# Kernel optimization log

Measured on AMD Instinct MI355X. Metric: run time of the kernel, lower is better.

## Reference

```python
import jax, jax.numpy as jnp
import numpy as np

B, W, CBLK, C, H, L, VOCAB = 8, 512, 24, 512, 8, 2, 256
HD = C // H


def _ln(x, g, b, eps=1e-5):
    m = x.mean(-1, keepdims=True)
    v = ((x - m) ** 2).mean(-1, keepdims=True)
    return (x - m) * jax.lax.rsqrt(v + eps) * g + b


def _causal_attn(q, k, v):
    # q,k,v: [..., T, hd]; causal softmax attention, scale 1/sqrt(hd)
    T = q.shape[-2]
    scale = 1.0 / (q.shape[-1] ** 0.5)
    s = jnp.einsum('...qd,...kd->...qk', q, k) * scale
    mask = jnp.tril(jnp.ones((T, T), dtype=bool))
    s = jnp.where(mask, s, jnp.finfo(s.dtype).min)
    return jnp.einsum('...qk,...kd->...qd', jax.nn.softmax(s, axis=-1), v)


def _mha_char(seq, w_qkv, last_ix):
    # seq: [B,W,c,C]; per-word causal char attention, then gather row last_ix
    b, w, c, _ = seq.shape
    q, k, v = jnp.split(seq @ w_qkv, 3, axis=-1)
    sh = lambda t: t.reshape(b, w, c, H, HD).transpose(0, 1, 3, 2, 4)
    o = _causal_attn(sh(q), sh(k), sh(v))          # [B,W,H,c,hd]
    o = o.transpose(0, 1, 3, 2, 4).reshape(b, w, c, C)
    return jnp.take_along_axis(o, last_ix[:, :, None, None], axis=2)[:, :, 0, :]


def _mha_word(x, w_qkv, w_proj):
    b, w, _ = x.shape
    q, k, v = jnp.split(x @ w_qkv, 3, axis=-1)
    sh = lambda t: t.reshape(b, w, H, HD).transpose(0, 2, 1, 3)
    o = _causal_attn(sh(q), sh(k), sh(v))
    o = o.transpose(0, 2, 1, 3).reshape(b, w, C)
    return o @ w_proj


def setup_inputs() -> dict:
    key = jax.random.key(0)
    ks = jax.random.split(key, 16)
    # ragged word lengths in [1, CBLK]; mask = ones then zeros (as produced by pad())
    lengths = jax.random.randint(ks[0], (B, W), 1, CBLK + 1)
    attention_mask = (jnp.arange(CBLK)[None, None, :] < lengths[:, :, None]).astype(jnp.int32)
    x = jax.random.randint(ks[1], (B, W, CBLK), 0, VOCAB).astype(jnp.int32)
    std = 0.02
    res_std = std * (2 * L) ** -0.5  # res_flag init scaling
    n = lambda k, s, sd=std: sd * jax.random.normal(k, s, dtype=jnp.float32)
    return dict(
        x=x, attention_mask=attention_mask,
        cte=n(ks[2], (VOCAB, C)), cpe=n(ks[3], (CBLK, C)), wpe=n(ks[4], (W, C)),
        ln1_g=jnp.ones((L, C)), ln1_b=jnp.zeros((L, C)),
        ln2_g=jnp.ones((L, C)), ln2_b=jnp.zeros((L, C)),
        ln3_g=jnp.ones((L, C)), ln3_b=jnp.zeros((L, C)),
        cattn_w=n(ks[5], (L, C, 3 * C)), cattn_proj=n(ks[6], (L, C, C)),
        wattn_w=n(ks[7], (L, C, 3 * C)), wattn_proj=n(ks[8], (L, C, C), res_std),
        mlp_fc=n(ks[9], (L, C, 4 * C)), mlp_proj=n(ks[10], (L, 4 * C, C), res_std),
        proj_w=n(ks[11], (C, CBLK * C)), lm_head_w=n(ks[12], (C, VOCAB)),
    )


def reference(x, attention_mask, cte, cpe, wpe, ln1_g, ln1_b, ln2_g, ln2_b, ln3_g, ln3_b,
              cattn_w, cattn_proj, wattn_w, wattn_proj, mlp_fc, mlp_proj, proj_w, lm_head_w):
    last_ix = attention_mask.sum(axis=2) - 1           # [B,W], last real char per word
    state = cte[x] + cpe[None, None, :, :]             # [B,W,c,C]
    context = None                                     # current_conv.context/pad, vectorized
    for l in range(L):
        if l == 0:
            # first_time: operate on full padded char sequences, cache ln_1 output
            hln = _ln(state, ln1_g[l], ln1_b[l])       # [B,W,c,C]
            context = hln
            seq = hln
        else:
            # splice the new word vector into position last_ix of the cached context
            hln = _ln(state, ln1_g[l], ln1_b[l])       # [B,W,C]
            repl = jnp.arange(CBLK)[None, None, :] == last_ix[:, :, None]
            seq = jnp.where(repl[..., None], hln[:, :, None, :], context)
        o = _mha_char(seq, cattn_w[l], last_ix)        # [B,W,C]
        if l == 0:
            o = o + wpe[None, :, :]                    # word pos emb added only first_time
        state = o @ cattn_proj[l]                      # note: no residual around c_attn
        state = state + _mha_word(_ln(state, ln2_g[l], ln2_b[l]), wattn_w[l], wattn_proj[l])
        hm = _ln(state, ln3_g[l], ln3_b[l])
        state = state + jax.nn.gelu(hm @ mlp_fc[l], approximate=False) @ mlp_proj[l]
    y = (state @ proj_w).reshape(B, W, CBLK, C)
    return y @ lm_head_w                               # logits [B,W,CBLK,VOCAB]
```

## Files before the change

### kernel.cpp

```cpp
#include <hip/hip_runtime.h>
#include <hip/hip_bf16.h>
#include <math.h>


namespace {

constexpr int Bn = 8, Wn = 512, CB = 24, Cd = 512, Hn = 8, Lln = 2, Vn = 256, HDn = 64;
constexpr int BW = Bn * Wn;
constexpr int C3 = 3 * Cd;
constexpr int FF = 4 * Cd;
constexpr int NROW = BW * CB;

typedef unsigned short u16;
typedef short short8 __attribute__((ext_vector_type(8)));
typedef float f32x4 __attribute__((ext_vector_type(4)));
typedef __attribute__((address_space(1))) void gvoid_t;
typedef __attribute__((address_space(3))) void lvoid_t;

__device__ __forceinline__ u16 f2bu(float f) {
  __hip_bfloat16 h = __float2bfloat16(f);
  return __builtin_bit_cast(u16, h);
}
__device__ __forceinline__ float bu2f(u16 u) {
  return __bfloat162float(__builtin_bit_cast(__hip_bfloat16, u));
}
__device__ __forceinline__ float geluf(float x) {
  return 0.5f * x * (1.0f + erff(x * 0.7071067811865475f));
}
__device__ __forceinline__ void gl16(const void* g, void* l) {
  __builtin_amdgcn_global_load_lds((gvoid_t*)g, (lvoid_t*)l, 16, 0, 0);
}

__global__ void k_lastix(const int* __restrict__ mask, int* __restrict__ lastix) {
  int i = blockIdx.x * 256 + threadIdx.x;
  if (i < BW) {
    int s = 0;
#pragma unroll
    for (int j = 0; j < CB; ++j) s += mask[i * CB + j];
    lastix[i] = s - 1;
  }
}

__device__ __forceinline__ void f2b8(const float* __restrict__ s, u16* __restrict__ d) {
  float4 a = *(const float4*)s;
  float4 b = *(const float4*)(s + 4);
  union { uint4 u; u16 h[8]; } pk;
  pk.h[0] = f2bu(a.x); pk.h[1] = f2bu(a.y); pk.h[2] = f2bu(a.z); pk.h[3] = f2bu(a.w);
  pk.h[4] = f2bu(b.x); pk.h[5] = f2bu(b.y); pk.h[6] = f2bu(b.z); pk.h[7] = f2bu(b.w);
  *(uint4*)d = pk.u;
}

__device__ __forceinline__ void wT_tile(const float* __restrict__ src, u16* __restrict__ dst,
                                        int K, int N, int n0, int k0,
                                        u16 T[64][72], int tid) {
  int kl = tid >> 2, nc = (tid & 3) * 16;
  const float* s = src + (long)(k0 + kl) * N + n0 + nc;
#pragma unroll
  for (int u = 0; u < 4; ++u) {
    float4 f = *(const float4*)(s + u * 4);
    T[nc + u * 4 + 0][kl] = f2bu(f.x);
    T[nc + u * 4 + 1][kl] = f2bu(f.y);
    T[nc + u * 4 + 2][kl] = f2bu(f.z);
    T[nc + u * 4 + 3][kl] = f2bu(f.w);
  }
  __syncthreads();
  int nl = tid >> 2, kc = (tid & 3) * 16;
  u16* d = dst + (long)(n0 + nl) * K + k0 + kc;
  *(uint4*)d = *(uint4*)&T[nl][kc];
  *(uint4*)(d + 8) = *(uint4*)&T[nl][kc + 8];
}

__global__ __launch_bounds__(256) void k_prep(
    const float* __restrict__ proj_w, u16* __restrict__ projwb,
    const float* __restrict__ cattn_w, u16* __restrict__ wcb,
    const float* __restrict__ lm_head, u16* __restrict__ lmhT,
    const float* __restrict__ cattn_proj, const float* __restrict__ wattn_w,
    const float* __restrict__ wattn_proj, const float* __restrict__ mlp_fc,
    const float* __restrict__ mlp_proj, u16* __restrict__ wT) {
  __shared__ u16 T[64][72];
  int b = blockIdx.x, tid = threadIdx.x;
  if (b < 3072) { long i = ((long)b * 256 + tid) * 8; f2b8(proj_w + i, projwb + i); return; }
  b -= 3072;
  if (b < 768) { long i = ((long)b * 256 + tid) * 8; f2b8(cattn_w + i, wcb + i); return; }
  b -= 768;
  if (b < 32) { wT_tile(lm_head, lmhT, Cd, Vn, (b & 3) * 64, (b >> 2) * 64, T, tid); return; }
  b -= 32;
  int l = b >> 10, r = b & 1023;
  size_t lw = (size_t)(2 * C3 * Cd + 2 * Cd * Cd + 2 * FF * Cd);
  u16* bl = wT + l * lw;
  const float* src; u16* dst; int K, N, nt;
  if (r < 192)      { src = cattn_w + (size_t)l * Cd * C3;    dst = bl;                              K = Cd; N = C3; nt = 24; }
  else if (r < 256) { src = cattn_proj + (size_t)l * Cd * Cd; dst = bl + C3 * Cd;                    K = Cd; N = Cd; nt = 8;  r -= 192; }
  else if (r < 448) { src = wattn_w + (size_t)l * Cd * C3;    dst = bl + C3 * Cd + Cd * Cd;          K = Cd; N = C3; nt = 24; r -= 256; }
  else if (r < 512) { src = wattn_proj + (size_t)l * Cd * Cd; dst = bl + 2 * C3 * Cd + Cd * Cd;      K = Cd; N = Cd; nt = 8;  r -= 448; }
  else if (r < 768) { src = mlp_fc + (size_t)l * Cd * FF;     dst = bl + 2 * C3 * Cd + 2 * Cd * Cd;  K = Cd; N = FF; nt = 32; r -= 512; }
  else              { src = mlp_proj + (size_t)l * FF * Cd;   dst = bl + 2 * C3 * Cd + 2 * Cd * Cd + FF * Cd; K = FF; N = Cd; nt = 8; r -= 768; }
  wT_tile(src, dst, K, N, (r % nt) * 64, (r / nt) * 64, T, tid);
}

__global__ __launch_bounds__(64) void k_embed_ln(
    const int* __restrict__ x, const float* __restrict__ cte, const float* __restrict__ cpe,
    const float* __restrict__ g, const float* __restrict__ b,
    const int* __restrict__ lastix, u16* __restrict__ ctx) {
  int r = blockIdx.x;
  int bw = r / CB, ch = r - bw * CB;
  if (ch > lastix[bw]) return;
  int tok = x[r];
  const float* e = cte + (long)tok * Cd;
  const float* pe = cpe + (long)ch * Cd;
  int lane = threadIdx.x;
  float v[8];
  float s = 0.f, sq = 0.f;
#pragma unroll
  for (int u = 0; u < 2; ++u) {
    float4 a = *(const float4*)(e + u * 256 + lane * 4);
    float4 p4 = *(const float4*)(pe + u * 256 + lane * 4);
    v[u * 4 + 0] = a.x + p4.x; v[u * 4 + 1] = a.y + p4.y;
    v[u * 4 + 2] = a.z + p4.z; v[u * 4 + 3] = a.w + p4.w;
  }
#pragma unroll
  for (int u = 0; u < 8; ++u) { s += v[u]; sq += v[u] * v[u]; }
#pragma unroll
  for (int m = 32; m; m >>= 1) { s += __shfl_xor(s, m); sq += __shfl_xor(sq, m); }
  float mean = s * (1.0f / Cd);
  float var = sq * (1.0f / Cd) - mean * mean;
  float rs = rsqrtf(var + 1e-5f);
  u16* o = ctx + (long)r * Cd;
#pragma unroll
  for (int u = 0; u < 2; ++u) {
    int c0 = u * 256 + lane * 4;
    float4 g4 = *(const float4*)(g + c0);
    float4 b4 = *(const float4*)(b + c0);
    float o0 = (v[u * 4 + 0] - mean) * rs * g4.x + b4.x;
    float o1 = (v[u * 4 + 1] - mean) * rs * g4.y + b4.y;
    float o2 = (v[u * 4 + 2] - mean) * rs * g4.z + b4.z;
    float o3 = (v[u * 4 + 3] - mean) * rs * g4.w + b4.w;
    uint2 w;
    w.x = (unsigned)f2bu(o0) | ((unsigned)f2bu(o1) << 16);
    w.y = (unsigned)f2bu(o2) | ((unsigned)f2bu(o3) << 16);
    *(uint2*)(o + c0) = w;
  }
}

__global__ __launch_bounds__(64) void k_ln(
    const float* __restrict__ X, u16* __restrict__ Y,
    const float* __restrict__ g, const float* __restrict__ b) {
  long r = blockIdx.x;
  const float* xr = X + r * Cd;
  int lane = threadIdx.x;
  float v[8];
  float s = 0.f, sq = 0.f;
#pragma unroll
  for (int u = 0; u < 2; ++u) {
    float4 a = *(const float4*)(xr + u * 256 + lane * 4);
    v[u * 4 + 0] = a.x; v[u * 4 + 1] = a.y; v[u * 4 + 2] = a.z; v[u * 4 + 3] = a.w;
  }
#pragma unroll
  for (int u = 0; u < 8; ++u) { s += v[u]; sq += v[u] * v[u]; }
#pragma unroll
  for (int m = 32; m; m >>= 1) { s += __shfl_xor(s, m); sq += __shfl_xor(sq, m); }
  float mean = s * (1.0f / Cd);
  float var = sq * (1.0f / Cd) - mean * mean;
  float rs = rsqrtf(var + 1e-5f);
  u16* o = Y + r * Cd;
#pragma unroll
  for (int u = 0; u < 2; ++u) {
    int c0 = u * 256 + lane * 4;
    float4 g4 = *(const float4*)(g + c0);
    float4 b4 = *(const float4*)(b + c0);
    float o0 = (v[u * 4 + 0] - mean) * rs * g4.x + b4.x;
    float o1 = (v[u * 4 + 1] - mean) * rs * g4.y + b4.y;
    float o2 = (v[u * 4 + 2] - mean) * rs * g4.z + b4.z;
    float o3 = (v[u * 4 + 3] - mean) * rs * g4.w + b4.w;
    uint2 w;
    w.x = (unsigned)f2bu(o0) | ((unsigned)f2bu(o1) << 16);
    w.y = (unsigned)f2bu(o2) | ((unsigned)f2bu(o3) << 16);
    *(uint2*)(o + c0) = w;
  }
}

__global__ __launch_bounds__(64) void k_gather_last(
    const u16* __restrict__ ctx, const int* __restrict__ lastix, u16* __restrict__ qin) {
  long bw = blockIdx.x;
  int r = (int)bw * CB + lastix[bw];
  const uint4* s = (const uint4*)(ctx + (long)r * Cd);
  uint4* d = (uint4*)(qin + bw * Cd);
  d[threadIdx.x] = s[threadIdx.x];
}

template <int BM, int BN, int EPI, int OUTBF>
__global__ __launch_bounds__(256) void k_mgemm(
    const u16* __restrict__ A, int lda, long sA1, long sA2,
    const u16* __restrict__ Bt, int ldb, long sB1, long sB2,
    void* __restrict__ Cv, int ldc, long sC1, long sC2,
    const float* __restrict__ R, u16* __restrict__ D2,
    const float* __restrict__ PL, const u16* __restrict__ VL,
    const float* __restrict__ WP, int K, int zdiv) {
  constexpr int WM = BM / 2;
  constexpr int WN = BN / 2;
  constexpr int FM = WM / 16, FN = WN / 16;
  __shared__ u16 As[BM * 32];
  __shared__ u16 Bs[BN * 32];
  long m0 = (long)blockIdx.y * BM, n0 = (long)blockIdx.x * BN;
  int z = blockIdx.z;
  int z1 = z / zdiv, z2 = z - z1 * zdiv;
  A += z1 * sA1 + z2 * sA2;
  Bt += z1 * sB1 + z2 * sB2;
  long coff = z1 * sC1 + z2 * sC2;
  int tid = threadIdx.x;
  int wid = tid >> 6, lane = tid & 63;
  int wr = wid >> 1, wc = wid & 1;

  const int srow = tid >> 2, skk = (tid & 3) * 8;
  const u16* Ald[BM / 64];
  const u16* Bld[BN / 64];
#pragma unroll
  for (int i = 0; i < BM / 64; ++i) Ald[i] = A + (m0 + srow + i * 64) * (long)lda + skk;
#pragma unroll
  for (int i = 0; i < BN / 64; ++i) Bld[i] = Bt + (n0 + srow + i * 64) * (long)ldb + skk;

  f32x4 acc[FM][FN] = {};
  const int fr = lane & 15, kg = lane >> 4;

  for (int k0 = 0; k0 < K; k0 += 32) {
#pragma unroll
    for (int i = 0; i < BM / 64; ++i) gl16(Ald[i] + k0, &As[(tid + i * 256) * 8]);
#pragma unroll
    for (int i = 0; i < BN / 64; ++i) gl16(Bld[i] + k0, &Bs[(tid + i * 256) * 8]);
    __syncthreads();
    short8 af[FM], bf[FN];
#pragma unroll
    for (int m = 0; m < FM; ++m)
      af[m] = *(const short8*)&As[(wr * WM + m * 16 + fr) * 32 + kg * 8];
#pragma unroll
    for (int n = 0; n < FN; ++n)
      bf[n] = *(const short8*)&Bs[(wc * WN + n * 16 + fr) * 32 + kg * 8];
#pragma unroll
    for (int m = 0; m < FM; ++m)
#pragma unroll
      for (int n = 0; n < FN; ++n)
        acc[m][n] = __builtin_amdgcn_mfma_f32_16x16x32_bf16(af[m], bf[n], acc[m][n], 0, 0, 0);
    __syncthreads();
  }
  int ccol = lane & 15, crow4 = (lane >> 4) * 4;
#pragma unroll
  for (int m = 0; m < FM; ++m)
#pragma unroll
    for (int n = 0; n < FN; ++n)
#pragma unroll
      for (int q = 0; q < 4; ++q) {
        long gr = m0 + wr * WM + m * 16 + crow4 + q;
        long gc = n0 + wc * WN + n * 16 + ccol;
        float v = acc[m][n][q];
        long idx = gr * (long)ldc + gc + coff;
        if (EPI == 1 || EPI == 3) v += R[idx];
        if (EPI == 2) v = geluf(v);
        if (EPI == 4) {
          v += PL[gr * 8 + z2] * bu2f(VL[gr * (long)C3 + 2 * Cd + z2 * 64 + gc]);
          if (WP) v += WP[(long)(gr & (Wn - 1)) * Cd + z2 * 64 + gc];
        }
        if (EPI == 3) {
          ((float*)Cv)[idx] = v;
          D2[idx] = f2bu(v);
        } else if (OUTBF) {
          ((u16*)Cv)[idx] = f2bu(v);
        } else {
          ((float*)Cv)[idx] = v;
        }
      }
}

__global__ __launch_bounds__(256) void k_cattn2(
    const u16* __restrict__ ctx, const u16* __restrict__ qtil,
    const u16* __restrict__ qkvc, const int* __restrict__ lastix,
    u16* __restrict__ U, float* __restrict__ plast) {
  int gw = blockIdx.x;
  int li = lastix[gw];
  __shared__ u16 ctxs[CB][512];
  __shared__ u16 qks[2][512];
  __shared__ float sp[Hn][CB];
  int tid = threadIdx.x;
  for (int u = tid; u < li * 64; u += 256) {
    int row = u >> 6, c = (u & 63) * 8;
    *(uint4*)&ctxs[row][c] = *(const uint4*)(ctx + ((long)(gw * CB + row)) * Cd + c);
  }
  if (tid < 128) {
    int row = tid >> 6, c = (tid & 63) * 8;
    *(uint4*)&qks[row][c] = *(const uint4*)(qkvc + (long)gw * C3 + row * 512 + c);
  }
  int wid = tid >> 6, lane = tid & 63;
  int h0 = wid * 2, h1 = h0 + 1;
  float q0[8], q1[8];
  {
    const u16* q0p = qtil + (long)gw * 4096 + h0 * 512 + lane * 8;
    uint4 a = *(const uint4*)q0p;
    uint4 b = *(const uint4*)(q0p + 512);
    const u16* qa = (const u16*)&a;
    const u16* qb = (const u16*)&b;
#pragma unroll
    for (int u = 0; u < 8; ++u) { q0[u] = bu2f(qa[u]); q1[u] = bu2f(qb[u]); }
  }
  __syncthreads();
  int j = 0;
  for (; j + 2 <= li; j += 2) {
    float p0a = 0.f, p1a = 0.f, p0b = 0.f, p1b = 0.f;
    const u16* cva = &ctxs[j][lane * 8];
    const u16* cvb = &ctxs[j + 1][lane * 8];
#pragma unroll
    for (int u = 0; u < 8; ++u) {
      float ca = bu2f(cva[u]);
      float cb = bu2f(cvb[u]);
      p0a += ca * q0[u]; p1a += ca * q1[u];
      p0b += cb * q0[u]; p1b += cb * q1[u];
    }
#pragma unroll
    for (int m = 32; m; m >>= 1) {
      p0a += __shfl_xor(p0a, m); p1a += __shfl_xor(p1a, m);
      p0b += __shfl_xor(p0b, m); p1b += __shfl_xor(p1b, m);
    }
    if (lane == 0) {
      sp[h0][j] = p0a * 0.125f; sp[h1][j] = p1a * 0.125f;
      sp[h0][j + 1] = p0b * 0.125f; sp[h1][j + 1] = p1b * 0.125f;
    }
  }
  if (j < li) {
    float p0 = 0.f, p1 = 0.f;
    const u16* cv = &ctxs[j][lane * 8];
#pragma unroll
    for (int u = 0; u < 8; ++u) {
      float c = bu2f(cv[u]);
      p0 += c * q0[u];
      p1 += c * q1[u];
    }
#pragma unroll
    for (int m = 32; m; m >>= 1) { p0 += __shfl_xor(p0, m); p1 += __shfl_xor(p1, m); }
    if (lane == 0) { sp[h0][j] = p0 * 0.125f; sp[h1][j] = p1 * 0.125f; }
  }
  {
    float pr = 0.f;
    const u16* qq = &qks[0][lane * 8];
    const u16* kk = &qks[1][lane * 8];
#pragma unroll
    for (int u = 0; u < 8; ++u) pr += bu2f(qq[u]) * bu2f(kk[u]);
    float a0 = ((lane >> 3) == h0) ? pr : 0.f;
    float a1 = ((lane >> 3) == h1) ? pr : 0.f;
#pragma unroll
    for (int m = 32; m; m >>= 1) { a0 += __shfl_xor(a0, m); a1 += __shfl_xor(a1, m); }
    if (lane == 0) { sp[h0][li] = a0 * 0.125f; sp[h1][li] = a1 * 0.125f; }
  }
  __syncthreads();
  if (tid < 8) {
    float m = -3.4e38f;
    for (int jj = 0; jj <= li; ++jj) m = fmaxf(m, sp[tid][jj]);
    float s = 0.f;
    for (int jj = 0; jj <= li; ++jj) { float e = expf(sp[tid][jj] - m); sp[tid][jj] = e; s += e; }
    float inv = 1.0f / s;
    for (int jj = 0; jj <= li; ++jj) sp[tid][jj] *= inv;
    plast[gw * 8 + tid] = sp[tid][li];
  }
  __syncthreads();
  int h = tid >> 5, d0 = (tid & 31) * 16;
  float uacc[16];
#pragma unroll
  for (int i = 0; i < 16; ++i) uacc[i] = 0.f;
  for (int jj = 0; jj < li; ++jj) {
    float p = sp[h][jj];
    const u16* cv = &ctxs[jj][d0];
#pragma unroll
    for (int i = 0; i < 16; ++i) uacc[i] += p * bu2f(cv[i]);
  }
  union { uint4 q[2]; u16 hh[16]; } pk;
#pragma unroll
  for (int i = 0; i < 16; ++i) pk.hh[i] = f2bu(uacc[i]);
  u16* d = U + (long)gw * 4096 + h * 512 + d0;
  *(uint4*)d = pk.q[0];
  *(uint4*)(d + 8) = pk.q[1];
}

__global__ __launch_bounds__(256) void k_vt(const u16* __restrict__ qkv, u16* __restrict__ Vt) {
  __shared__ u16 T[64][72];
  int z = blockIdx.y, jt = blockIdx.x;
  int b = z >> 3, h = z & 7;
  int tid = threadIdx.x;
  int jl = tid >> 2, dc = (tid & 3) * 16;
  const u16* s = qkv + ((long)(b * Wn + jt * 64 + jl)) * C3 + 2 * Cd + h * HDn + dc;
  *(uint4*)&T[jl][dc] = *(const uint4*)s;
  *(uint4*)&T[jl][dc + 8] = *(const uint4*)(s + 8);
  __syncthreads();
  int dl = tid >> 2, jc = (tid & 3) * 16;
  u16 tmp[16];
#pragma unroll
  for (int u = 0; u < 16; ++u) tmp[u] = T[jc + u][dl];
  u16* d = Vt + (long)z * HDn * Wn + (long)dl * Wn + jt * 64 + jc;
  *(uint4*)d = *(uint4*)&tmp[0];
  *(uint4*)(d + 8) = *(uint4*)&tmp[8];
}

__global__ __launch_bounds__(256) void k_fattn(
    const u16* __restrict__ qkv, const u16* __restrict__ Vt, u16* __restrict__ ao) {
  constexpr int ST = 68;
  __shared__ u16 Ks[64 * ST];
  __shared__ u16 Vs[64 * ST];
  __shared__ u16 Ps[4][16 * ST];
  int qt = blockIdx.x;
  int z  = blockIdx.y;
  int b = z >> 3, h = z & 7;
  int tid = threadIdx.x;
  int w = tid >> 6, lane = tid & 63;
  int fr = lane & 15, kg = lane >> 4;

  short8 qf[2];
  {
    const u16* qp = qkv + ((long)(b * Wn + qt * 64 + w * 16 + fr)) * C3 + h * 64 + kg * 8;
    qf[0] = *(const short8*)qp;
    qf[1] = *(const short8*)(qp + 32);
  }
  f32x4 oacc[4] = {};
  float mrow[4], lrow[4];
#pragma unroll
  for (int q = 0; q < 4; ++q) { mrow[q] = -3.4e38f; lrow[q] = 0.f; }

  for (int kt = 0; kt <= qt; ++kt) {
    __syncthreads();
    {
      int r = tid >> 2, c = (tid & 3) * 16;
      const u16* kp = qkv + ((long)(b * Wn + kt * 64 + r)) * C3 + Cd + h * 64 + c;
      *(uint4*)&Ks[r * ST + c] = *(const uint4*)kp;
      *(uint4*)&Ks[r * ST + c + 8] = *(const uint4*)(kp + 8);
      const u16* vp = Vt + (long)z * (64 * Wn) + (long)r * Wn + kt * 64 + c;
      *(uint4*)&Vs[r * ST + c] = *(const uint4*)vp;
      *(uint4*)&Vs[r * ST + c + 8] = *(const uint4*)(vp + 8);
    }
    __syncthreads();
    f32x4 s[4];
#pragma unroll
    for (int n = 0; n < 4; ++n) {
      short8 kf0 = *(const short8*)&Ks[(n * 16 + fr) * ST + kg * 8];
      short8 kf1 = *(const short8*)&Ks[(n * 16 + fr) * ST + kg * 8 + 32];
      f32x4 a = {};
      a = __builtin_amdgcn_mfma_f32_16x16x32_bf16(qf[0], kf0, a, 0, 0, 0);
      a = __builtin_amdgcn_mfma_f32_16x16x32_bf16(qf[1], kf1, a, 0, 0, 0);
      s[n] = a;
    }
    int irow0 = qt * 64 + w * 16 + kg * 4;
#pragma unroll
    for (int n = 0; n < 4; ++n) {
      int jcol = kt * 64 + n * 16 + fr;
#pragma unroll
      for (int q = 0; q < 4; ++q) {
        float v = s[n][q] * 0.125f;
        s[n][q] = (jcol > irow0 + q) ? -3.4e38f : v;
      }
    }
    float sf[4];
#pragma unroll
    for (int q = 0; q < 4; ++q) {
      float mm = fmaxf(fmaxf(s[0][q], s[1][q]), fmaxf(s[2][q], s[3][q]));
      mm = fmaxf(mm, __shfl_xor(mm, 1));
      mm = fmaxf(mm, __shfl_xor(mm, 2));
      mm = fmaxf(mm, __shfl_xor(mm, 4));
      mm = fmaxf(mm, __shfl_xor(mm, 8));
      float mnew = fmaxf(mrow[q], mm);
      sf[q] = expf(mrow[q] - mnew);
      mrow[q] = mnew;
    }
    float ls[4] = {0.f, 0.f, 0.f, 0.f};
#pragma unroll
    for (int n = 0; n < 4; ++n) {
#pragma unroll
      for (int q = 0; q < 4; ++q) {
        float p = expf(s[n][q] - mrow[q]);
        u16 pb = f2bu(p);
        ls[q] += bu2f(pb);
        Ps[w][(kg * 4 + q) * ST + n * 16 + fr] = pb;
      }
    }
#pragma unroll
    for (int q = 0; q < 4; ++q) {
      float l = ls[q];
      l += __shfl_xor(l, 1); l += __shfl_xor(l, 2);
      l += __shfl_xor(l, 4); l += __shfl_xor(l, 8);
      lrow[q] = lrow[q] * sf[q] + l;
#pragma unroll
      for (int n = 0; n < 4; ++n) oacc[n][q] *= sf[q];
    }
    asm volatile("s_waitcnt lgkmcnt(0)" ::: "memory");
    short8 pa0 = *(const short8*)&Ps[w][fr * ST + kg * 8];
    short8 pa1 = *(const short8*)&Ps[w][fr * ST + kg * 8 + 32];
#pragma unroll
    for (int n = 0; n < 4; ++n) {
      short8 vf0 = *(const short8*)&Vs[(n * 16 + fr) * ST + kg * 8];
      short8 vf1 = *(const short8*)&Vs[(n * 16 + fr) * ST + kg * 8 + 32];
      oacc[n] = __builtin_amdgcn_mfma_f32_16x16x32_bf16(pa0, vf0, oacc[n], 0, 0, 0);
      oacc[n] = __builtin_amdgcn_mfma_f32_16x16x32_bf16(pa1, vf1, oacc[n], 0, 0, 0);
    }
  }
  int orow = b * Wn + qt * 64 + w * 16 + kg * 4;
#pragma unroll
  for (int q = 0; q < 4; ++q) {
    float inv = 1.0f / lrow[q];
#pragma unroll
    for (int n = 0; n < 4; ++n)
      ao[(long)(orow + q) * Cd + h * 64 + n * 16 + fr] = f2bu(oacc[n][q] * inv);
  }
}

template <int BM, int BN, int EPI, int OUTBF>
static inline void mgemm(hipStream_t st,
    const u16* A, int lda, long sA1, long sA2,
    const u16* Bt, int ldb, long sB1, long sB2,
    void* C, int ldc, long sC1, long sC2,
    const float* R, int M, int N, int K, int nz, int zdiv,
    u16* D2 = nullptr, const float* PL = nullptr, const u16* VL = nullptr,
    const float* WP = nullptr) {
  dim3 g(N / BN, (M + BM - 1) / BM, nz);
  hipLaunchKernelGGL((k_mgemm<BM, BN, EPI, OUTBF>), g, dim3(256), 0, st,
                     A, lda, sA1, sA2, Bt, ldb, sB1, sB2, C, ldc, sC1, sC2,
                     R ? R : (const float*)C, D2, PL, VL, WP, K, zdiv);
}

}

extern "C" void kernel_launch(void* const* d_in, const int* in_sizes, int n_in,
                              void* d_out, int out_size, void* d_ws, size_t ws_size,
                              hipStream_t stream) {
  (void)in_sizes; (void)n_in; (void)out_size; (void)ws_size;
  const int*   x          = (const int*)d_in[0];
  const int*   amask      = (const int*)d_in[1];
  const float* cte        = (const float*)d_in[2];
  const float* cpe        = (const float*)d_in[3];
  const float* wpe        = (const float*)d_in[4];
  const float* ln1g       = (const float*)d_in[5];
  const float* ln1b       = (const float*)d_in[6];
  const float* ln2g       = (const float*)d_in[7];
  const float* ln2b       = (const float*)d_in[8];
  const float* ln3g       = (const float*)d_in[9];
  const float* ln3b       = (const float*)d_in[10];
  const float* cattn_w    = (const float*)d_in[11];
  const float* cattn_proj = (const float*)d_in[12];
  const float* wattn_w    = (const float*)d_in[13];
  const float* wattn_proj = (const float*)d_in[14];
  const float* mlp_fc     = (const float*)d_in[15];
  const float* mlp_proj   = (const float*)d_in[16];
  const float* proj_w     = (const float*)d_in[17];
  const float* lm_head    = (const float*)d_in[18];
  float* out = (float*)d_out;

  char* base = (char*)d_ws;
  size_t off = 0;
  auto alloc = [&](size_t bytes) -> char* {
    char* r = base + off;
    off += (bytes + 255) & ~(size_t)255;
    return r;
  };
  int*   lastix = (int*)alloc((size_t)BW * 4);
  float* plast  = (float*)alloc((size_t)BW * 8 * 4);
  u16*   ctx    = (u16*)alloc((size_t)NROW * Cd * 2);
  char*  big    = alloc((size_t)105 * 1024 * 1024);
  u16*   kvq    = (u16*)alloc((size_t)BW * C3 * 2);
  u16*   qin    = (u16*)alloc((size_t)BW * Cd * 2);
  float* state  = (float*)alloc((size_t)BW * Cd * 4);
  u16*   stateb = (u16*)alloc((size_t)BW * Cd * 2);
  u16*   hln    = (u16*)alloc((size_t)BW * Cd * 2);
  u16*   ao     = (u16*)alloc((size_t)BW * Cd * 2);
  u16*   wT     = (u16*)alloc((size_t)2 * (2 * C3 * Cd + 2 * Cd * Cd + 2 * FF * Cd) * 2);
  u16*   wcb    = (u16*)alloc((size_t)2 * Cd * C3 * 2);
  u16*   projwb = (u16*)alloc((size_t)Cd * CB * Cd * 2);
  u16*   lmhT   = (u16*)alloc((size_t)Vn * Cd * 2);

  u16*   U     = (u16*)big;
  u16*   qtil  = (u16*)(big + (size_t)35651584);
  u16*   Vt    = (u16*)(big + (size_t)71303168);
  u16*   mlph  = (u16*)big;
  u16*   combT = (u16*)big;

  size_t lw = (size_t)(2 * C3 * Cd + 2 * Cd * Cd + 2 * FF * Cd);
  auto cwT    = [&](int l) { return wT + l * lw; };
  auto cprojT = [&](int l) { return wT + l * lw + C3 * Cd; };
  auto wwT    = [&](int l) { return wT + l * lw + C3 * Cd + Cd * Cd; };
  auto wprojT = [&](int l) { return wT + l * lw + 2 * C3 * Cd + Cd * Cd; };
  auto fcT    = [&](int l) { return wT + l * lw + 2 * C3 * Cd + 2 * Cd * Cd; };
  auto mprojT = [&](int l) { return wT + l * lw + 2 * C3 * Cd + 2 * Cd * Cd + FF * Cd; };

  hipLaunchKernelGGL(k_lastix, dim3(16), dim3(256), 0, stream, amask, lastix);
  hipLaunchKernelGGL(k_prep, dim3(5920), dim3(256), 0, stream,
                     proj_w, projwb, cattn_w, wcb, lm_head, lmhT,
                     cattn_proj, wattn_w, wattn_proj, mlp_fc, mlp_proj, wT);
  hipLaunchKernelGGL(k_embed_ln, dim3(NROW), dim3(64), 0, stream,
                     x, cte, cpe, ln1g, ln1b, lastix, ctx);

  for (int l = 0; l < Lln; ++l) {
    u16* qkvc = kvq;
    u16* qkvw = kvq;
    if (l == 0)
      hipLaunchKernelGGL(k_gather_last, dim3(BW), dim3(64), 0, stream, ctx, lastix, qin);
    else
      hipLaunchKernelGGL(k_ln, dim3(BW), dim3(64), 0, stream, state, qin, ln1g + Cd, ln1b + Cd);
    mgemm<128, 64, 0, 1>(stream, qin, Cd, 0, 0, cwT(l), Cd, 0, 0,
                         qkvc, C3, 0, 0, nullptr, BW, C3, Cd, 1, 1);
    mgemm<64, 64, 0, 1>(stream, qkvc, C3, 0, 64,
                        wcb + (size_t)l * Cd * C3 + Cd, C3, 0, 64,
                        qtil, 8 * Cd, 0, Cd, nullptr, BW, Cd, HDn, 8, 8);
    hipLaunchKernelGGL(k_cattn2, dim3(BW), dim3(256), 0, stream,
                       ctx, qtil, qkvc, lastix, U, plast);
    mgemm<64, 64, 4, 1>(stream, U, 8 * Cd, 0, Cd,
                        cwT(l) + (size_t)(2 * Cd) * Cd, Cd, 0, (long)HDn * Cd,
                        ao, Cd, 0, HDn, nullptr, BW, HDn, Cd, 8, 8,
                        nullptr, plast, qkvc, l == 0 ? wpe : nullptr);
    mgemm<64, 64, 0, 0>(stream, ao, Cd, 0, 0, cprojT(l), Cd, 0, 0,
                        state, Cd, 0, 0, nullptr, BW, Cd, Cd, 1, 1);
    hipLaunchKernelGGL(k_ln, dim3(BW), dim3(64), 0, stream, state, hln, ln2g + l * Cd, ln2b + l * Cd);
    mgemm<128, 64, 0, 1>(stream, hln, Cd, 0, 0, wwT(l), Cd, 0, 0,
                         qkvw, C3, 0, 0, nullptr, BW, C3, Cd, 1, 1);
    hipLaunchKernelGGL(k_vt, dim3(Wn / 64, 64), dim3(256), 0, stream, qkvw, Vt);
    hipLaunchKernelGGL(k_fattn, dim3(8, 64), dim3(256), 0, stream, qkvw, Vt, ao);
    mgemm<64, 64, 1, 0>(stream, ao, Cd, 0, 0, wprojT(l), Cd, 0, 0,
                        state, Cd, 0, 0, state, BW, Cd, Cd, 1, 1);
    hipLaunchKernelGGL(k_ln, dim3(BW), dim3(64), 0, stream, state, hln, ln3g + l * Cd, ln3b + l * Cd);
    mgemm<128, 128, 2, 1>(stream, hln, Cd, 0, 0, fcT(l), Cd, 0, 0,
                          mlph, FF, 0, 0, nullptr, BW, FF, Cd, 1, 1);
    mgemm<64, 64, 3, 0>(stream, mlph, FF, 0, 0, mprojT(l), FF, 0, 0,
                        state, Cd, 0, 0, state, BW, Cd, FF, 1, 1, stateb);
  }

  mgemm<64, 64, 0, 1>(stream, lmhT, Cd, 0, 0,
                      projwb, CB * Cd, 0, Cd,
                      combT, Cd, 0, (long)Vn * Cd,
                      nullptr, Vn, Cd, Cd, CB, CB);
  mgemm<128, 128, 0, 0>(stream, stateb, Cd, 0, 0, combT, Cd, 0, 0,
                        out, CB * Vn, 0, 0, nullptr, BW, CB * Vn, Cd, 1, 1);
}
```

Baseline: 578.8 us.

## Split-K the MLP down-projection into four partials plus reduction kernel

The MLP projection GEMM (K=2048) is split into four K=512 slices via the batched z dimension, writing fp32 partials to a scratch buffer, and a new reduction kernel sums them into the residual state and emits the bf16 copy. This raises block count for a GEMM with a small output (4096x512), improving occupancy at the cost of extra global traffic for the partials. Separately, the char-attention kernel drops the shared-memory staging of the q/k last-row pair and computes the self score with 8 threads reading global memory directly, which shrinks shared memory.

```diff
diff --git a/kernel.cpp b/kernel.cpp
--- a/kernel.cpp
+++ b/kernel.cpp
@@ -188,6 +188,23 @@
   d[threadIdx.x] = s[threadIdx.x];
 }
 
+__global__ __launch_bounds__(256) void k_red4(const float* __restrict__ pbuf,
+                                              float* __restrict__ state,
+                                              u16* __restrict__ stateb) {
+  long i = ((long)blockIdx.x * 256 + threadIdx.x) * 4;
+  float4 a = *(const float4*)(state + i);
+#pragma unroll
+  for (int z = 0; z < 4; ++z) {
+    float4 p = *(const float4*)(pbuf + (long)z * BW * Cd + i);
+    a.x += p.x; a.y += p.y; a.z += p.z; a.w += p.w;
+  }
+  *(float4*)(state + i) = a;
+  uint2 w;
+  w.x = (unsigned)f2bu(a.x) | ((unsigned)f2bu(a.y) << 16);
+  w.y = (unsigned)f2bu(a.z) | ((unsigned)f2bu(a.w) << 16);
+  *(uint2*)(stateb + i) = w;
+}
+
 template <int BM, int BN, int EPI, int OUTBF>
 __global__ __launch_bounds__(256) void k_mgemm(
     const u16* __restrict__ A, int lda, long sA1, long sA2,
@@ -276,17 +293,12 @@
     u16* __restrict__ U, float* __restrict__ plast) {
   int gw = blockIdx.x;
   int li = lastix[gw];
-  __shared__ u16 ctxs[CB][512];
-  __shared__ u16 qks[2][512];
+  __shared__ u16 ctxs[CB - 1][512];
   __shared__ float sp[Hn][CB];
   int tid = threadIdx.x;
   for (int u = tid; u < li * 64; u += 256) {
     int row = u >> 6, c = (u & 63) * 8;
     *(uint4*)&ctxs[row][c] = *(const uint4*)(ctx + ((long)(gw * CB + row)) * Cd + c);
-  }
-  if (tid < 128) {
-    int row = tid >> 6, c = (tid & 63) * 8;
-    *(uint4*)&qks[row][c] = *(const uint4*)(qkvc + (long)gw * C3 + row * 512 + c);
   }
   int wid = tid >> 6, lane = tid & 63;
   int h0 = wid * 2, h1 = h0 + 1;
@@ -336,17 +348,13 @@
     for (int m = 32; m; m >>= 1) { p0 += __shfl_xor(p0, m); p1 += __shfl_xor(p1, m); }
     if (lane == 0) { sp[h0][j] = p0 * 0.125f; sp[h1][j] = p1 * 0.125f; }
   }
-  {
-    float pr = 0.f;
-    const u16* qq = &qks[0][lane * 8];
-    const u16* kk = &qks[1][lane * 8];
-#pragma unroll
-    for (int u = 0; u < 8; ++u) pr += bu2f(qq[u]) * bu2f(kk[u]);
-    float a0 = ((lane >> 3) == h0) ? pr : 0.f;
-    float a1 = ((lane >> 3) == h1) ? pr : 0.f;
-#pragma unroll
-    for (int m = 32; m; m >>= 1) { a0 += __shfl_xor(a0, m); a1 += __shfl_xor(a1, m); }
-    if (lane == 0) { sp[h0][li] = a0 * 0.125f; sp[h1][li] = a1 * 0.125f; }
+  if (tid < 8) {
+    const u16* qq = qkvc + (long)gw * C3 + tid * 64;
+    const u16* kk = qq + Cd;
+    float s = 0.f;
+#pragma unroll
+    for (int u = 0; u < 64; ++u) s += bu2f(qq[u]) * bu2f(kk[u]);
+    sp[tid][li] = s * 0.125f;
   }
   __syncthreads();
   if (tid < 8) {
@@ -572,6 +580,7 @@
   u16*   qtil  = (u16*)(big + (size_t)35651584);
   u16*   Vt    = (u16*)(big + (size_t)71303168);
   u16*   mlph  = (u16*)big;
+  float* pbuf  = (float*)(big + (size_t)50 * 1024 * 1024);
   u16*   combT = (u16*)big;
 
   size_t lw = (size_t)(2 * C3 * Cd + 2 * Cd * Cd + 2 * FF * Cd);
@@ -619,8 +628,12 @@
     hipLaunchKernelGGL(k_ln, dim3(BW), dim3(64), 0, stream, state, hln, ln3g + l * Cd, ln3b + l * Cd);
     mgemm<128, 128, 2, 1>(stream, hln, Cd, 0, 0, fcT(l), Cd, 0, 0,
                           mlph, FF, 0, 0, nullptr, BW, FF, Cd, 1, 1);
-    mgemm<64, 64, 3, 0>(stream, mlph, FF, 0, 0, mprojT(l), FF, 0, 0,
-                        state, Cd, 0, 0, state, BW, Cd, FF, 1, 1, stateb);
+    mgemm<64, 64, 0, 0>(stream, mlph, FF, 0, 512,
+                        mprojT(l), FF, 0, 512,
+                        pbuf, Cd, 0, (long)BW * Cd,
+                        nullptr, BW, Cd, 512, 4, 4);
+    hipLaunchKernelGGL(k_red4, dim3((BW * Cd) / 1024), dim3(256), 0, stream,
+                       pbuf, state, stateb);
   }
 
   mgemm<64, 64, 0, 1>(stream, lmhT, Cd, 0, 0,
```

New measurement: 588.3 us. No clear change (+1.6%).

## Compute char-attention scores with MFMA and shrink MLP fc GEMM tile

Applied to the files above, without the earlier changes.

The score computation in the per-word char attention kernel moves from per-lane scalar dot products with shuffle reductions to bf16 MFMA 16x16x32 instructions. Each wave covers a 128-wide slice of the 8 heads and writes partial scores to LDS, where they are summed across waves. The context rows are stored with a padded stride, and the q·k term for the last position is now a plain 64-element loop run by 8 threads. Separately, the MLP fc GEMM tile drops from 128x128 to 64x64 to launch more blocks, at the cost of less reuse per block.

```diff
diff --git a/kernel.cpp b/kernel.cpp
--- a/kernel.cpp
+++ b/kernel.cpp
@@ -274,79 +274,57 @@
     const u16* __restrict__ ctx, const u16* __restrict__ qtil,
     const u16* __restrict__ qkvc, const int* __restrict__ lastix,
     u16* __restrict__ U, float* __restrict__ plast) {
+  constexpr int CS = 520;
   int gw = blockIdx.x;
   int li = lastix[gw];
-  __shared__ u16 ctxs[CB][512];
-  __shared__ u16 qks[2][512];
+  __shared__ u16 ctxs[CB - 1][CS];
+  __shared__ float spf[4][Hn][32];
   __shared__ float sp[Hn][CB];
   int tid = threadIdx.x;
   for (int u = tid; u < li * 64; u += 256) {
     int row = u >> 6, c = (u & 63) * 8;
     *(uint4*)&ctxs[row][c] = *(const uint4*)(ctx + ((long)(gw * CB + row)) * Cd + c);
   }
-  if (tid < 128) {
-    int row = tid >> 6, c = (tid & 63) * 8;
-    *(uint4*)&qks[row][c] = *(const uint4*)(qkvc + (long)gw * C3 + row * 512 + c);
-  }
-  int wid = tid >> 6, lane = tid & 63;
-  int h0 = wid * 2, h1 = h0 + 1;
-  float q0[8], q1[8];
+  __syncthreads();
+  int w = tid >> 6, lane = tid & 63;
+  int fr = lane & 15, kg = lane >> 4;
   {
-    const u16* q0p = qtil + (long)gw * 4096 + h0 * 512 + lane * 8;
-    uint4 a = *(const uint4*)q0p;
-    uint4 b = *(const uint4*)(q0p + 512);
-    const u16* qa = (const u16*)&a;
-    const u16* qb = (const u16*)&b;
-#pragma unroll
-    for (int u = 0; u < 8; ++u) { q0[u] = bu2f(qa[u]); q1[u] = bu2f(qb[u]); }
+    const u16* qbase = qtil + (long)gw * 4096 + (fr & 7) * 512 + w * 128 + kg * 8;
+    int r0 = fr;
+    int r1 = 16 + fr; if (r1 > CB - 2) r1 = CB - 2;
+    f32x4 acc0 = {}, acc1 = {};
+#pragma unroll
+    for (int kk = 0; kk < 4; ++kk) {
+      short8 af = *(const short8*)(qbase + kk * 32);
+      short8 b0 = *(const short8*)&ctxs[r0][w * 128 + kk * 32 + kg * 8];
+      short8 b1 = *(const short8*)&ctxs[r1][w * 128 + kk * 32 + kg * 8];
+      acc0 = __builtin_amdgcn_mfma_f32_16x16x32_bf16(af, b0, acc0, 0, 0, 0);
+      acc1 = __builtin_amdgcn_mfma_f32_16x16x32_bf16(af, b1, acc1, 0, 0, 0);
+    }
+    if (lane < 32) {
+      int jj = lane & 15;
+#pragma unroll
+      for (int q = 0; q < 4; ++q) {
+        int h = (lane >> 4) * 4 + q;
+        spf[w][h][jj] = acc0[q];
+        spf[w][h][16 + jj] = acc1[q];
+      }
+    }
   }
   __syncthreads();
-  int j = 0;
-  for (; j + 2 <= li; j += 2) {
-    float p0a = 0.f, p1a = 0.f, p0b = 0.f, p1b = 0.f;
-    const u16* cva = &ctxs[j][lane * 8];
-    const u16* cvb = &ctxs[j + 1][lane * 8];
-#pragma unroll
-    for (int u = 0; u < 8; ++u) {
-      float ca = bu2f(cva[u]);
-      float cb = bu2f(cvb[u]);
-      p0a += ca * q0[u]; p1a += ca * q1[u];
-      p0b += cb * q0[u]; p1b += cb * q1[u];
-    }
-#pragma unroll
-    for (int m = 32; m; m >>= 1) {
-      p0a += __shfl_xor(p0a, m); p1a += __shfl_xor(p1a, m);
-      p0b += __shfl_xor(p0b, m); p1b += __shfl_xor(p1b, m);
-    }
-    if (lane == 0) {
-      sp[h0][j] = p0a * 0.125f; sp[h1][j] = p1a * 0.125f;
-      sp[h0][j + 1] = p0b * 0.125f; sp[h1][j + 1] = p1b * 0.125f;
-    }
-  }
-  if (j < li) {
-    float p0 = 0.f, p1 = 0.f;
-    const u16* cv = &ctxs[j][lane * 8];
-#pragma unroll
-    for (int u = 0; u < 8; ++u) {
-      float c = bu2f(cv[u]);
-      p0 += c * q0[u];
-      p1 += c * q1[u];
-    }
-#pragma unroll
-    for (int m = 32; m; m >>= 1) { p0 += __shfl_xor(p0, m); p1 += __shfl_xor(p1, m); }
-    if (lane == 0) { sp[h0][j] = p0 * 0.125f; sp[h1][j] = p1 * 0.125f; }
-  }
   {
-    float pr = 0.f;
-    const u16* qq = &qks[0][lane * 8];
-    const u16* kk = &qks[1][lane * 8];
-#pragma unroll
-    for (int u = 0; u < 8; ++u) pr += bu2f(qq[u]) * bu2f(kk[u]);
-    float a0 = ((lane >> 3) == h0) ? pr : 0.f;
-    float a1 = ((lane >> 3) == h1) ? pr : 0.f;
-#pragma unroll
-    for (int m = 32; m; m >>= 1) { a0 += __shfl_xor(a0, m); a1 += __shfl_xor(a1, m); }
-    if (lane == 0) { sp[h0][li] = a0 * 0.125f; sp[h1][li] = a1 * 0.125f; }
+    int h = tid >> 5, j = tid & 31;
+    if (j < CB)
+      sp[h][j] = (spf[0][h][j] + spf[1][h][j] + spf[2][h][j] + spf[3][h][j]) * 0.125f;
+  }
+  __syncthreads();
+  if (tid < 8) {
+    const u16* qq = qkvc + (long)gw * C3 + tid * 64;
+    const u16* kk = qq + Cd;
+    float s = 0.f;
+#pragma unroll
+    for (int u = 0; u < 64; ++u) s += bu2f(qq[u]) * bu2f(kk[u]);
+    sp[tid][li] = s * 0.125f;
   }
   __syncthreads();
   if (tid < 8) {
@@ -617,8 +595,8 @@
     mgemm<64, 64, 1, 0>(stream, ao, Cd, 0, 0, wprojT(l), Cd, 0, 0,
                         state, Cd, 0, 0, state, BW, Cd, Cd, 1, 1);
     hipLaunchKernelGGL(k_ln, dim3(BW), dim3(64), 0, stream, state, hln, ln3g + l * Cd, ln3b + l * Cd);
-    mgemm<128, 128, 2, 1>(stream, hln, Cd, 0, 0, fcT(l), Cd, 0, 0,
-                          mlph, FF, 0, 0, nullptr, BW, FF, Cd, 1, 1);
+    mgemm<64, 64, 2, 1>(stream, hln, Cd, 0, 0, fcT(l), Cd, 0, 0,
+                        mlph, FF, 0, 0, nullptr, BW, FF, Cd, 1, 1);
     mgemm<64, 64, 3, 0>(stream, mlph, FF, 0, 0, mprojT(l), FF, 0, 0,
                         state, Cd, 0, 0, state, BW, Cd, FF, 1, 1, stateb);
   }
```

After: 543.6 us. 6.1% less time.
